# Kernel optimization log

Measured on AMD Instinct MI355X. Metric: run time of the kernel, lower is better.

Reference implementation:

```python
import jax, jax.numpy as jnp
import numpy as np


def setup_inputs() -> dict:
    key = jax.random.key(0)
    k1, k2 = jax.random.split(key)
    N, M, Q, D = 4096, 128, 64, 128
    a_embeddings = jax.random.normal(k1, (N, D), dtype=jnp.float32)
    b_embedding_sets = jax.random.normal(k2, (M, Q, D), dtype=jnp.float32)
    gaussian_variance = jnp.full((1,), 0.5, dtype=jnp.float32)  # nn.Parameter default
    return {
        "a_embeddings": a_embeddings,
        "b_embedding_sets": b_embedding_sets,
        "gaussian_variance": gaussian_variance,
    }


def reference(a_embeddings, b_embedding_sets, gaussian_variance):
    # Covariance = var * I, so inv(cov) = I / var and the Mahalanobis term is
    # ||a - mu||^2 / var. Expand the squared distance to avoid the NxMxQxD
    # broadcast intermediate the torch code materializes (same math).
    inv_var = 1.0 / gaussian_variance[0]
    a2 = jnp.sum(a_embeddings * a_embeddings, axis=-1)          # [N]
    b2 = jnp.sum(b_embedding_sets * b_embedding_sets, axis=-1)  # [M, Q]
    ab = jnp.einsum("nd,mqd->nmq", a_embeddings, b_embedding_sets)  # [N, M, Q]
    x2 = (a2[:, None, None] - 2.0 * ab + b2[None, :, :]) * inv_var  # [N, M, Q]
    densities = jnp.exp(-0.5 * x2)                  # [N, M, Q]
    dens_per_cluster = densities.sum(axis=2)        # [N, M]
    prob = dens_per_cluster / (dens_per_cluster.sum(axis=1, keepdims=True) + 1e-10)
    return prob
```

## Files before the change

kernel.cpp:

```cpp
#include <hip/hip_runtime.h>
#include <math.h>

#define NN 4096
#define MM 128
#define QQ 64
#define DD 128
#define CC (MM * QQ)
#define GRIDN 512

typedef float f32x4 __attribute__((ext_vector_type(4)));
typedef int   i32x4 __attribute__((ext_vector_type(4)));
typedef int   i32x8 __attribute__((ext_vector_type(8)));

#define AS1 __attribute__((address_space(1)))
#define AS3 __attribute__((address_space(3)))

__device__ __forceinline__ void grid_barrier(unsigned* base, int bid)
{
    __syncthreads();
    asm volatile("" ::: "memory");
    if (threadIdx.x == 0) {
        unsigned* sub    = base + (bid & 7) * 16;
        unsigned* master = base + 240;
        const unsigned prev =
            __hip_atomic_fetch_add(sub, 1u, __ATOMIC_RELAXED, __HIP_MEMORY_SCOPE_AGENT);
        if (prev == 63u)
            __hip_atomic_fetch_add(master, 1u, __ATOMIC_RELAXED, __HIP_MEMORY_SCOPE_AGENT);
        while (__hip_atomic_load(master, __ATOMIC_RELAXED, __HIP_MEMORY_SCOPE_AGENT) < 8u)
            __builtin_amdgcn_s_sleep(8);
    }
    asm volatile("" ::: "memory");
    __syncthreads();
}

__global__ __launch_bounds__(256, 2)
void kde_fused(const float* __restrict__ A, const float* __restrict__ B,
               const float* __restrict__ var,
               unsigned char* __restrict__ A8, unsigned char* __restrict__ B8,
               float* __restrict__ a2w, float* __restrict__ b2w,
               float* __restrict__ dpc,
               float* __restrict__ out,
               unsigned* __restrict__ bar)
{
    __shared__ unsigned char Bs[128 * DD];
    __shared__ unsigned char As[2][128 * DD];
    __shared__ float a2s[2][128];
    __shared__ float b2s[128];

    const int bid = blockIdx.x;
    const int t = threadIdx.x, w = t >> 6, lane = t & 63;

    {
        const int l32 = t & 31;
        #pragma unroll
        for (int p = 0; p < 3; ++p) {
            const int row = bid * 24 + p * 8 + (t >> 5);
            const float* src; unsigned char* dst; float* nrm;
            if (row < NN) { src = A + (size_t)row * DD; dst = A8 + (size_t)row * DD; nrm = a2w + row; }
            else {
                const int r = row - NN;
                src = B + (size_t)r * DD; dst = B8 + (size_t)r * DD; nrm = b2w + r;
            }
            const float4 v = ((const float4*)src)[l32];
            int pk = __builtin_amdgcn_cvt_pk_fp8_f32(v.x, v.y, 0, false);
            pk     = __builtin_amdgcn_cvt_pk_fp8_f32(v.z, v.w, pk, true);
            __hip_atomic_store((unsigned int*)dst + l32, (unsigned int)pk,
                               __ATOMIC_RELAXED, __HIP_MEMORY_SCOPE_AGENT);
            float s = v.x * v.x + v.y * v.y + v.z * v.z + v.w * v.w;
            #pragma unroll
            for (int mth = 16; mth > 0; mth >>= 1) s += __shfl_xor(s, mth, 64);
            if (l32 == 0)
                __hip_atomic_store(nrm, s, __ATOMIC_RELAXED, __HIP_MEMORY_SCOPE_AGENT);
        }
    }

    grid_barrier(bar, bid);

    {
        const int xcd = bid & 7;
        const int cb  = (xcd << 3) | ((bid >> 3) & 7);
        const int nb0 = bid >> 6;
        const int c0  = cb * 128;

        {
            const unsigned char* Bb = B8 + (size_t)c0 * DD;
            #pragma unroll
            for (int i = 0; i < 4; ++i) {
                const int slot = w * 256 + i * 64 + lane;
                const int r = slot >> 3, c16 = slot & 7, scb = c16 ^ (r & 7);
                __builtin_amdgcn_global_load_lds(
                    (const AS1 unsigned int*)(Bb + r * DD + scb * 16),
                    (AS3 unsigned int*)&Bs[slot * 16], 16, 0, 0);
            }
            if (w >= 2)
                __builtin_amdgcn_global_load_lds(
                    (const AS1 unsigned int*)(b2w + c0 + (w - 2) * 64 + lane),
                    (AS3 unsigned int*)&b2s[(w - 2) * 64 + lane], 4, 0, 0);
            const int n0 = nb0 * 128;
            const unsigned char* Ab = A8 + (size_t)n0 * DD;
            #pragma unroll
            for (int i = 0; i < 4; ++i) {
                const int slot = w * 256 + i * 64 + lane;
                const int r = slot >> 3, c16 = slot & 7, scb = c16 ^ (r & 7);
                __builtin_amdgcn_global_load_lds(
                    (const AS1 unsigned int*)(Ab + r * DD + scb * 16),
                    (AS3 unsigned int*)&As[0][slot * 16], 16, 0, 0);
            }
            if (w < 2)
                __builtin_amdgcn_global_load_lds(
                    (const AS1 unsigned int*)(a2w + n0 + w * 64 + lane),
                    (AS3 unsigned int*)&a2s[0][w * 64 + lane], 4, 0, 0);
        }
        __syncthreads();

        const int l15 = lane & 15, q = lane >> 4, xr = l15 & 7;
        const int wy = w >> 1, wx = w & 1;
        const int rbase = wy * 64, cbase = wx * 64;
        const int m = (cb << 1) + wx;
        const float hinv = 0.5f / var[0];
        const float h2   = hinv + hinv;

        f32x4 nbh[4];
        #pragma unroll
        for (int jc = 0; jc < 4; ++jc) {
            const f32x4 bv = *(const f32x4*)&b2s[cbase + jc * 16 + q * 4];
            nbh[jc] = -bv * hinv;
        }

        #pragma unroll
        for (int t4 = 0; t4 < 4; ++t4) {
            const int buf = t4 & 1;
            const int n0  = (nb0 + 8 * t4) * 128;

            if (t4 < 3) {
                const int n0n = (nb0 + 8 * (t4 + 1)) * 128;
                const unsigned char* Ab = A8 + (size_t)n0n * DD;
                #pragma unroll
                for (int i = 0; i < 4; ++i) {
                    const int slot = w * 256 + i * 64 + lane;
                    const int r = slot >> 3, c16 = slot & 7, scb = c16 ^ (r & 7);
                    __builtin_amdgcn_global_load_lds(
                        (const AS1 unsigned int*)(Ab + r * DD + scb * 16),
                        (AS3 unsigned int*)&As[buf ^ 1][slot * 16], 16, 0, 0);
                }
                if (w < 2)
                    __builtin_amdgcn_global_load_lds(
                        (const AS1 unsigned int*)(a2w + n0n + w * 64 + lane),
                        (AS3 unsigned int*)&a2s[buf ^ 1][w * 64 + lane], 4, 0, 0);
            }

            i32x8 a8[4];
            #pragma unroll
            for (int i = 0; i < 4; ++i) {
                const int ro = (rbase + i * 16 + l15) * DD;
                const i32x4 lo = *(const i32x4*)&As[buf][ro + (((q << 1) | 0) ^ xr) * 16];
                const i32x4 hi = *(const i32x4*)&As[buf][ro + (((q << 1) | 1) ^ xr) * 16];
                #pragma unroll
                for (int e = 0; e < 4; ++e) { a8[i][e] = lo[e]; a8[i][4 + e] = hi[e]; }
            }

            f32x4 acc[4][4] = {};
            __builtin_amdgcn_s_setprio(1);
            #pragma unroll
            for (int jc = 0; jc < 4; ++jc) {
                const int ro = (cbase + jc * 16 + l15) * DD;
                const i32x4 lo = *(const i32x4*)&Bs[ro + (((q << 1) | 0) ^ xr) * 16];
                const i32x4 hi = *(const i32x4*)&Bs[ro + (((q << 1) | 1) ^ xr) * 16];
                i32x8 b8;
                #pragma unroll
                for (int e = 0; e < 4; ++e) { b8[e] = lo[e]; b8[4 + e] = hi[e]; }
                #pragma unroll
                for (int i = 0; i < 4; ++i)
                    acc[jc][i] = __builtin_amdgcn_mfma_scale_f32_16x16x128_f8f6f4(
                                    b8, a8[i], acc[jc][i],
                                    0, 0,
                                    0, 127,
                                    0, 127);
            }
            __builtin_amdgcn_s_setprio(0);

            float sums[4];
            #pragma unroll
            for (int i = 0; i < 4; ++i) {
                const float aih = a2s[buf][rbase + i * 16 + l15] * hinv;
                float s = 0.f;
                #pragma unroll
                for (int jc = 0; jc < 4; ++jc)
                    #pragma unroll
                    for (int r = 0; r < 4; ++r)
                        s += __expf(fmaf(h2, acc[jc][i][r], nbh[jc][r] - aih));
                s += __shfl_xor(s, 16, 64);
                s += __shfl_xor(s, 32, 64);
                sums[i] = s;
            }
            const float v01 = (q & 1) ? sums[1] : sums[0];
            const float v23 = (q & 1) ? sums[3] : sums[2];
            const float myv = (q & 2) ? v23 : v01;
            __hip_atomic_store(&dpc[(size_t)m * NN + n0 + rbase + lane], myv,
                               __ATOMIC_RELAXED, __HIP_MEMORY_SCOPE_AGENT);
            __syncthreads();
        }
    }

    grid_barrier(bar + 256, bid);

    {
        const int n0c = bid * 8;
        float* tile = (float*)&As[0][0];
        float* rden = b2s;
        const int mr = t >> 1, half = t & 1;
        const float4 v = *(const float4*)&dpc[(size_t)mr * NN + n0c + half * 4];
        float* tr = &tile[mr * 9 + half * 4];
        tr[0] = v.x; tr[1] = v.y; tr[2] = v.z; tr[3] = v.w;
        __syncthreads();
        if (t < 8) {
            float s = 0.f;
            #pragma unroll 8
            for (int mm = 0; mm < MM; ++mm) s += tile[mm * 9 + t];
            rden[t] = 1.f / (s + 1e-10f);
        }
        __syncthreads();
        const int j = t >> 5, mq = (t & 31) * 4;
        const float r = rden[j];
        float4 o;
        o.x = tile[(mq + 0) * 9 + j] * r;
        o.y = tile[(mq + 1) * 9 + j] * r;
        o.z = tile[(mq + 2) * 9 + j] * r;
        o.w = tile[(mq + 3) * 9 + j] * r;
        *(float4*)&out[(size_t)(n0c + j) * MM + mq] = o;
    }
}

extern "C" void kernel_launch(void* const* d_in, const int* in_sizes, int n_in,
                              void* d_out, int out_size, void* d_ws, size_t ws_size,
                              hipStream_t stream) {
    const float* A   = (const float*)d_in[0];
    const float* B   = (const float*)d_in[1];
    const float* var = (const float*)d_in[2];
    float* out = (float*)d_out;

    unsigned char* A8 = (unsigned char*)d_ws;
    unsigned char* B8 = A8 + (size_t)NN * DD;
    float* a2  = (float*)(B8 + (size_t)CC * DD);
    float* b2  = a2 + NN;
    float* dpc = b2 + CC;
    unsigned* bar = (unsigned*)((char*)d_ws + (4u << 20));

    hipMemsetAsync(bar, 0, 2048, stream);
    kde_fused<<<GRIDN, 256, 0, stream>>>(A, B, var, A8, B8, a2, b2, dpc, out, bar);
}
```

Measured before the change: 80.19 us.

## Convert fp32 tiles to fp8 in-block, drop pre-pass barrier and memset

Each block now loads its fp32 B and A tiles straight from global memory, converts them to fp8 and computes row norms into LDS itself. This removes the global fp8 workspace, the first grid-wide barrier and the separate memset launch. The grid barrier now uses persistent device-global counters with generation-based targets, so it no longer needs resetting. In exchange each A/B tile is converted redundantly by many blocks, and the A prefetch becomes register-staged fp32 loads (64 extra VGPRs) converted after the exp phase instead of async global-to-LDS copies.

After: 90.10 us. +12.4%, slower.

```diff
diff --git a/kernel.cpp b/kernel.cpp
--- a/kernel.cpp
+++ b/kernel.cpp
@@ -15,18 +15,22 @@
 #define AS1 __attribute__((address_space(1)))
 #define AS3 __attribute__((address_space(3)))
 
-__device__ __forceinline__ void grid_barrier(unsigned* base, int bid)
+__device__ unsigned g_sub[8 * 16];
+__device__ unsigned g_master;
+
+__device__ __forceinline__ void grid_barrier(int bid)
 {
     __syncthreads();
     asm volatile("" ::: "memory");
     if (threadIdx.x == 0) {
-        unsigned* sub    = base + (bid & 7) * 16;
-        unsigned* master = base + 240;
+        unsigned* sub = &g_sub[(bid & 7) * 16];
         const unsigned prev =
             __hip_atomic_fetch_add(sub, 1u, __ATOMIC_RELAXED, __HIP_MEMORY_SCOPE_AGENT);
-        if (prev == 63u)
-            __hip_atomic_fetch_add(master, 1u, __ATOMIC_RELAXED, __HIP_MEMORY_SCOPE_AGENT);
-        while (__hip_atomic_load(master, __ATOMIC_RELAXED, __HIP_MEMORY_SCOPE_AGENT) < 8u)
+        const unsigned tgt = ((prev >> 6) + 1u) << 3;
+        if ((prev & 63u) == 63u)
+            __hip_atomic_fetch_add(&g_master, 1u, __ATOMIC_RELAXED, __HIP_MEMORY_SCOPE_AGENT);
+        while ((int)(__hip_atomic_load(&g_master, __ATOMIC_RELAXED,
+                                       __HIP_MEMORY_SCOPE_AGENT) - tgt) < 0)
             __builtin_amdgcn_s_sleep(8);
     }
     asm volatile("" ::: "memory");
@@ -36,11 +40,8 @@
 __global__ __launch_bounds__(256, 2)
 void kde_fused(const float* __restrict__ A, const float* __restrict__ B,
                const float* __restrict__ var,
-               unsigned char* __restrict__ A8, unsigned char* __restrict__ B8,
-               float* __restrict__ a2w, float* __restrict__ b2w,
                float* __restrict__ dpc,
-               float* __restrict__ out,
-               unsigned* __restrict__ bar)
+               float* __restrict__ out)
 {
     __shared__ unsigned char Bs[128 * DD];
     __shared__ unsigned char As[2][128 * DD];
@@ -50,159 +51,124 @@
     const int bid = blockIdx.x;
     const int t = threadIdx.x, w = t >> 6, lane = t & 63;
 
-    {
-        const int l32 = t & 31;
-        #pragma unroll
-        for (int p = 0; p < 3; ++p) {
-            const int row = bid * 24 + p * 8 + (t >> 5);
-            const float* src; unsigned char* dst; float* nrm;
-            if (row < NN) { src = A + (size_t)row * DD; dst = A8 + (size_t)row * DD; nrm = a2w + row; }
-            else {
-                const int r = row - NN;
-                src = B + (size_t)r * DD; dst = B8 + (size_t)r * DD; nrm = b2w + r;
+    const int xcd = bid & 7;
+    const int cb  = (xcd << 3) | ((bid >> 3) & 7);
+    const int nb0 = bid >> 6;
+    const int c0  = cb * 128;
+
+    const int rr = t >> 1, hh = t & 1;
+    float4 vv[16];
+
+    auto load_tile = [&](const float* __restrict__ src) {
+        const float4* s4 = (const float4*)src;
+        const int base = (rr << 5) + (hh << 4);
+        #pragma unroll
+        for (int f = 0; f < 16; ++f) vv[f] = s4[base + f];
+    };
+    auto convert_tile = [&](unsigned char* __restrict__ dst, float* __restrict__ nrm) {
+        float s = 0.f;
+        #pragma unroll
+        for (int i = 0; i < 4; ++i) {
+            i32x4 wvv;
+            #pragma unroll
+            for (int k = 0; k < 4; ++k) {
+                const float4 v = vv[i * 4 + k];
+                s += v.x * v.x + v.y * v.y + v.z * v.z + v.w * v.w;
+                int pk = __builtin_amdgcn_cvt_pk_fp8_f32(v.x, v.y, 0, false);
+                pk     = __builtin_amdgcn_cvt_pk_fp8_f32(v.z, v.w, pk, true);
+                wvv[k] = pk;
             }
-            const float4 v = ((const float4*)src)[l32];
-            int pk = __builtin_amdgcn_cvt_pk_fp8_f32(v.x, v.y, 0, false);
-            pk     = __builtin_amdgcn_cvt_pk_fp8_f32(v.z, v.w, pk, true);
-            __hip_atomic_store((unsigned int*)dst + l32, (unsigned int)pk,
-                               __ATOMIC_RELAXED, __HIP_MEMORY_SCOPE_AGENT);
-            float s = v.x * v.x + v.y * v.y + v.z * v.z + v.w * v.w;
-            #pragma unroll
-            for (int mth = 16; mth > 0; mth >>= 1) s += __shfl_xor(s, mth, 64);
-            if (l32 == 0)
-                __hip_atomic_store(nrm, s, __ATOMIC_RELAXED, __HIP_MEMORY_SCOPE_AGENT);
-        }
-    }
-
-    grid_barrier(bar, bid);
-
-    {
-        const int xcd = bid & 7;
-        const int cb  = (xcd << 3) | ((bid >> 3) & 7);
-        const int nb0 = bid >> 6;
-        const int c0  = cb * 128;
-
-        {
-            const unsigned char* Bb = B8 + (size_t)c0 * DD;
-            #pragma unroll
-            for (int i = 0; i < 4; ++i) {
-                const int slot = w * 256 + i * 64 + lane;
-                const int r = slot >> 3, c16 = slot & 7, scb = c16 ^ (r & 7);
-                __builtin_amdgcn_global_load_lds(
-                    (const AS1 unsigned int*)(Bb + r * DD + scb * 16),
-                    (AS3 unsigned int*)&Bs[slot * 16], 16, 0, 0);
-            }
-            if (w >= 2)
-                __builtin_amdgcn_global_load_lds(
-                    (const AS1 unsigned int*)(b2w + c0 + (w - 2) * 64 + lane),
-                    (AS3 unsigned int*)&b2s[(w - 2) * 64 + lane], 4, 0, 0);
-            const int n0 = nb0 * 128;
-            const unsigned char* Ab = A8 + (size_t)n0 * DD;
-            #pragma unroll
-            for (int i = 0; i < 4; ++i) {
-                const int slot = w * 256 + i * 64 + lane;
-                const int r = slot >> 3, c16 = slot & 7, scb = c16 ^ (r & 7);
-                __builtin_amdgcn_global_load_lds(
-                    (const AS1 unsigned int*)(Ab + r * DD + scb * 16),
-                    (AS3 unsigned int*)&As[0][slot * 16], 16, 0, 0);
-            }
-            if (w < 2)
-                __builtin_amdgcn_global_load_lds(
-                    (const AS1 unsigned int*)(a2w + n0 + w * 64 + lane),
-                    (AS3 unsigned int*)&a2s[0][w * 64 + lane], 4, 0, 0);
-        }
+            const int c16 = (hh << 2) | i;
+            *(i32x4*)&dst[((rr << 3) | (c16 ^ (rr & 7))) << 4] = wvv;
+        }
+        s += __shfl_xor(s, 1, 64);
+        if (hh == 0) nrm[rr] = s;
+    };
+
+    load_tile(B + (size_t)c0 * DD);
+    convert_tile(Bs, b2s);
+    load_tile(A + (size_t)(nb0 * 128) * DD);
+    convert_tile(As[0], a2s[0]);
+    __syncthreads();
+
+    const int l15 = lane & 15, q = lane >> 4, xr = l15 & 7;
+    const int wy = w >> 1, wx = w & 1;
+    const int rbase = wy * 64, cbase = wx * 64;
+    const int m = (cb << 1) + wx;
+    const float hinv = 0.5f / var[0];
+    const float h2   = hinv + hinv;
+
+    f32x4 nbh[4];
+    #pragma unroll
+    for (int jc = 0; jc < 4; ++jc) {
+        const f32x4 bv = *(const f32x4*)&b2s[cbase + jc * 16 + q * 4];
+        nbh[jc] = -bv * hinv;
+    }
+
+    #pragma unroll
+    for (int t4 = 0; t4 < 4; ++t4) {
+        const int buf = t4 & 1;
+        const int n0  = (nb0 + 8 * t4) * 128;
+
+        if (t4 < 3)
+            load_tile(A + (size_t)((nb0 + 8 * (t4 + 1)) * 128) * DD);
+
+        i32x8 a8[4];
+        #pragma unroll
+        for (int i = 0; i < 4; ++i) {
+            const int ro = (rbase + i * 16 + l15) * DD;
+            const i32x4 lo = *(const i32x4*)&As[buf][ro + (((q << 1) | 0) ^ xr) * 16];
+            const i32x4 hi = *(const i32x4*)&As[buf][ro + (((q << 1) | 1) ^ xr) * 16];
+            #pragma unroll
+            for (int e = 0; e < 4; ++e) { a8[i][e] = lo[e]; a8[i][4 + e] = hi[e]; }
+        }
+
+        f32x4 acc[4][4] = {};
+        __builtin_amdgcn_s_setprio(1);
+        #pragma unroll
+        for (int jc = 0; jc < 4; ++jc) {
+            const int ro = (cbase + jc * 16 + l15) * DD;
+            const i32x4 lo = *(const i32x4*)&Bs[ro + (((q << 1) | 0) ^ xr) * 16];
+            const i32x4 hi = *(const i32x4*)&Bs[ro + (((q << 1) | 1) ^ xr) * 16];
+            i32x8 b8;
+            #pragma unroll
+            for (int e = 0; e < 4; ++e) { b8[e] = lo[e]; b8[4 + e] = hi[e]; }
+            #pragma unroll
+            for (int i = 0; i < 4; ++i)
+                acc[jc][i] = __builtin_amdgcn_mfma_scale_f32_16x16x128_f8f6f4(
+                                b8, a8[i], acc[jc][i],
+                                0, 0,
+                                0, 127,
+                                0, 127);
+        }
+        __builtin_amdgcn_s_setprio(0);
+
+        float sums[4];
+        #pragma unroll
+        for (int i = 0; i < 4; ++i) {
+            const float aih = a2s[buf][rbase + i * 16 + l15] * hinv;
+            float s = 0.f;
+            #pragma unroll
+            for (int jc = 0; jc < 4; ++jc)
+                #pragma unroll
+                for (int r = 0; r < 4; ++r)
+                    s += __expf(fmaf(h2, acc[jc][i][r], nbh[jc][r] - aih));
+            s += __shfl_xor(s, 16, 64);
+            s += __shfl_xor(s, 32, 64);
+            sums[i] = s;
+        }
+        const float v01 = (q & 1) ? sums[1] : sums[0];
+        const float v23 = (q & 1) ? sums[3] : sums[2];
+        const float myv = (q & 2) ? v23 : v01;
+        __hip_atomic_store(&dpc[(size_t)m * NN + n0 + rbase + lane], myv,
+                           __ATOMIC_RELAXED, __HIP_MEMORY_SCOPE_AGENT);
+
+        if (t4 < 3)
+            convert_tile(As[buf ^ 1], a2s[buf ^ 1]);
         __syncthreads();
-
-        const int l15 = lane & 15, q = lane >> 4, xr = l15 & 7;
-        const int wy = w >> 1, wx = w & 1;
-        const int rbase = wy * 64, cbase = wx * 64;
-        const int m = (cb << 1) + wx;
-        const float hinv = 0.5f / var[0];
-        const float h2   = hinv + hinv;
-
-        f32x4 nbh[4];
-        #pragma unroll
-        for (int jc = 0; jc < 4; ++jc) {
-            const f32x4 bv = *(const f32x4*)&b2s[cbase + jc * 16 + q * 4];
-            nbh[jc] = -bv * hinv;
-        }
-
-        #pragma unroll
-        for (int t4 = 0; t4 < 4; ++t4) {
-            const int buf = t4 & 1;
-            const int n0  = (nb0 + 8 * t4) * 128;
-
-            if (t4 < 3) {
-                const int n0n = (nb0 + 8 * (t4 + 1)) * 128;
-                const unsigned char* Ab = A8 + (size_t)n0n * DD;
-                #pragma unroll
-                for (int i = 0; i < 4; ++i) {
-                    const int slot = w * 256 + i * 64 + lane;
-                    const int r = slot >> 3, c16 = slot & 7, scb = c16 ^ (r & 7);
-                    __builtin_amdgcn_global_load_lds(
-                        (const AS1 unsigned int*)(Ab + r * DD + scb * 16),
-                        (AS3 unsigned int*)&As[buf ^ 1][slot * 16], 16, 0, 0);
-                }
-                if (w < 2)
-                    __builtin_amdgcn_global_load_lds(
-                        (const AS1 unsigned int*)(a2w + n0n + w * 64 + lane),
-                        (AS3 unsigned int*)&a2s[buf ^ 1][w * 64 + lane], 4, 0, 0);
-            }
-
-            i32x8 a8[4];
-            #pragma unroll
-            for (int i = 0; i < 4; ++i) {
-                const int ro = (rbase + i * 16 + l15) * DD;
-                const i32x4 lo = *(const i32x4*)&As[buf][ro + (((q << 1) | 0) ^ xr) * 16];
-                const i32x4 hi = *(const i32x4*)&As[buf][ro + (((q << 1) | 1) ^ xr) * 16];
-                #pragma unroll
-                for (int e = 0; e < 4; ++e) { a8[i][e] = lo[e]; a8[i][4 + e] = hi[e]; }
-            }
-
-            f32x4 acc[4][4] = {};
-            __builtin_amdgcn_s_setprio(1);
-            #pragma unroll
-            for (int jc = 0; jc < 4; ++jc) {
-                const int ro = (cbase + jc * 16 + l15) * DD;
-                const i32x4 lo = *(const i32x4*)&Bs[ro + (((q << 1) | 0) ^ xr) * 16];
-                const i32x4 hi = *(const i32x4*)&Bs[ro + (((q << 1) | 1) ^ xr) * 16];
-                i32x8 b8;
-                #pragma unroll
-                for (int e = 0; e < 4; ++e) { b8[e] = lo[e]; b8[4 + e] = hi[e]; }
-                #pragma unroll
-                for (int i = 0; i < 4; ++i)
-                    acc[jc][i] = __builtin_amdgcn_mfma_scale_f32_16x16x128_f8f6f4(
-                                    b8, a8[i], acc[jc][i],
-                                    0, 0,
-                                    0, 127,
-                                    0, 127);
-            }
-            __builtin_amdgcn_s_setprio(0);
-
-            float sums[4];
-            #pragma unroll
-            for (int i = 0; i < 4; ++i) {
-                const float aih = a2s[buf][rbase + i * 16 + l15] * hinv;
-                float s = 0.f;
-                #pragma unroll
-                for (int jc = 0; jc < 4; ++jc)
-                    #pragma unroll
-                    for (int r = 0; r < 4; ++r)
-                        s += __expf(fmaf(h2, acc[jc][i][r], nbh[jc][r] - aih));
-                s += __shfl_xor(s, 16, 64);
-                s += __shfl_xor(s, 32, 64);
-                sums[i] = s;
-            }
-            const float v01 = (q & 1) ? sums[1] : sums[0];
-            const float v23 = (q & 1) ? sums[3] : sums[2];
-            const float myv = (q & 2) ? v23 : v01;
-            __hip_atomic_store(&dpc[(size_t)m * NN + n0 + rbase + lane], myv,
-                               __ATOMIC_RELAXED, __HIP_MEMORY_SCOPE_AGENT);
-            __syncthreads();
-        }
-    }
-
-    grid_barrier(bar + 256, bid);
+    }
+
+    grid_barrier(bid);
 
     {
         const int n0c = bid * 8;
@@ -239,13 +205,7 @@
     const float* var = (const float*)d_in[2];
     float* out = (float*)d_out;
 
-    unsigned char* A8 = (unsigned char*)d_ws;
-    unsigned char* B8 = A8 + (size_t)NN * DD;
-    float* a2  = (float*)(B8 + (size_t)CC * DD);
-    float* b2  = a2 + NN;
-    float* dpc = b2 + CC;
-    unsigned* bar = (unsigned*)((char*)d_ws + (4u << 20));
-
-    hipMemsetAsync(bar, 0, 2048, stream);
-    kde_fused<<<GRIDN, 256, 0, stream>>>(A, B, var, A8, B8, a2, b2, dpc, out, bar);
+    float* dpc = (float*)d_ws;
+
+    kde_fused<<<GRIDN, 256, 0, stream>>>(A, B, var, dpc, out);
 }
```
